# Kernel optimization log

Hardware: AMD Instinct MI355X
Metric: run time of the kernel (lower is better)

The kernel has to match this reference:

```python
import jax, jax.numpy as jnp
import numpy as np

COORD = 2
C_IN = 64
C_OUT = 4
PROJ_HID = 256
N_LAT = 4096
N_QRY = 16384
B = 4
E0 = 262144
E1 = 524288
KERNEL_DIMS = [2 * COORD, 64, 64, C_IN]  # LinearChannelMLP layers for the GNO kernel


def _init_linear(key, d_in, d_out):
    kw, kb = jax.random.split(key)
    scale = 1.0 / np.sqrt(d_in)
    W = jax.random.uniform(kw, (d_in, d_out), jnp.float32, -scale, scale)
    b = jax.random.uniform(kb, (d_out,), jnp.float32, -scale, scale)
    return W, b


def setup_inputs() -> dict:
    key = jax.random.key(0)
    ks = jax.random.split(key, 16)
    inp = {
        "latent_tokens_coord": jax.random.uniform(ks[0], (N_LAT, COORD), jnp.float32),
        "rndata": jax.random.normal(ks[1], (B, N_LAT, C_IN), jnp.float32),
        "query_coord": jax.random.uniform(ks[2], (N_QRY, COORD), jnp.float32),
        "src0": jax.random.randint(ks[3], (E0,), 0, N_LAT, jnp.int32),
        "qry0": jnp.sort(jax.random.randint(ks[4], (E0,), 0, N_QRY, jnp.int32)),
        "src1": jax.random.randint(ks[5], (E1,), 0, N_LAT, jnp.int32),
        "qry1": jnp.sort(jax.random.randint(ks[6], (E1,), 0, N_QRY, jnp.int32)),
    }
    # GNO kernel MLP (shared across scales): 4 -> 64 -> 64 -> 64, GELU between layers
    for i in range(3):
        W, b = _init_linear(ks[7 + i], KERNEL_DIMS[i], KERNEL_DIMS[i + 1])
        inp[f"Wk{i}"], inp[f"bk{i}"] = W, b
    # scale-weighting MLP: coord_dim -> 16 -> num_scales, softmax over scales
    inp["Wsw0"], inp["bsw0"] = _init_linear(ks[10], COORD, 16)
    inp["Wsw1"], inp["bsw1"] = _init_linear(ks[11], 16, 2)
    # projection ChannelMLP: in_channels -> 256 -> out_channels, GELU between
    inp["Wp0"], inp["bp0"] = _init_linear(ks[12], C_IN, PROJ_HID)
    inp["Wp1"], inp["bp1"] = _init_linear(ks[13], PROJ_HID, C_OUT)
    return inp


def _kernel_mlp(feat, Wk0, bk0, Wk1, bk1, Wk2, bk2):
    h = jax.nn.gelu(feat @ Wk0 + bk0)
    h = jax.nn.gelu(h @ Wk1 + bk1)
    return h @ Wk2 + bk2  # [E, C_IN]


def _gno_scale(latent_coord, query_coord, rndata, src, qry,
               Wk0, bk0, Wk1, bk1, Wk2, bk2):
    # gather per-edge coords: agg = cat(y_j, x_i) -> kernel MLP -> linear transform k * f_y
    feat = jnp.concatenate([latent_coord[src], query_coord[qry]], axis=-1)  # [E, 2*COORD]
    k = _kernel_mlp(feat, Wk0, bk0, Wk1, bk1, Wk2, bk2)                     # [E, C_IN]
    fy = rndata[:, src, :]                                                  # [B, E, C_IN]
    m = (k[None, :, :] * fy).transpose(1, 0, 2)                             # [E, B, C_IN]
    s = jax.ops.segment_sum(m, qry, num_segments=N_QRY)                     # [Q, B, C_IN]
    cnt = jax.ops.segment_sum(jnp.ones_like(qry, dtype=m.dtype), qry, num_segments=N_QRY)
    mean = s / jnp.maximum(cnt, 1.0)[:, None, None]                         # mean reduction
    return mean.transpose(1, 0, 2)                                          # [B, Q, C_IN]


def reference(latent_tokens_coord, rndata, query_coord,
              src0, qry0, src1, qry1,
              Wk0, bk0, Wk1, bk1, Wk2, bk2,
              Wsw0, bsw0, Wsw1, bsw1,
              Wp0, bp0, Wp1, bp1):
    d0 = _gno_scale(latent_tokens_coord, query_coord, rndata, src0, qry0,
                    Wk0, bk0, Wk1, bk1, Wk2, bk2)
    d1 = _gno_scale(latent_tokens_coord, query_coord, rndata, src1, qry1,
                    Wk0, bk0, Wk1, bk1, Wk2, bk2)
    # scale weights from query coords: softmax over scales
    h = jax.nn.relu(query_coord @ Wsw0 + bsw0)
    w = jax.nn.softmax(h @ Wsw1 + bsw1, axis=-1)          # [Q, 2]
    decoded = w[None, :, 0, None] * d0 + w[None, :, 1, None] * d1  # [B, Q, C_IN]
    # projection ChannelMLP (pointwise over nodes)
    out = jax.nn.gelu(decoded @ Wp0 + bp0) @ Wp1 + bp1    # [B, Q, C_OUT]
    return out
```

## Files before the change

kernel.cpp:

```cpp
#include <hip/hip_runtime.h>
#include <hip/hip_bf16.h>
#include <cstdint>

#define NLAT 4096
#define NQRY 16384
#define QPW  2
#define HSTR 68

#define WSYNC() asm volatile("s_waitcnt lgkmcnt(0)" ::: "memory")

typedef __attribute__((ext_vector_type(8))) short bh8;
typedef __attribute__((ext_vector_type(4))) float f32x4;

union FI { int i[4]; bh8 v; };

__device__ __forceinline__ float gelu_f(float x) {
    float x3 = x * x * x;
    float u2 = 1.5957691216057308f * (x + 0.044715f * x3);
    float r  = __builtin_amdgcn_rcpf(__expf(u2) + 1.0f);
    return x * (1.0f - r);
}

__device__ __forceinline__ int lower_bound(const int* __restrict__ a, int n, int v) {
    int lo = 0, hi = n;
    while (lo < hi) { int m = (lo + hi) >> 1; if (a[m] < v) lo = m + 1; else hi = m; }
    return lo;
}

__device__ __forceinline__ int pk(float a, float b) {
    return (int)__builtin_amdgcn_perm(__float_as_uint(b), __float_as_uint(a), 0x07060302u);
}

__device__ __forceinline__ void make_afrags(const float* sh, int lane, FI ah[2], FI al[2]) {
    const int m = lane & 15, quad = lane >> 4;
#pragma unroll
    for (int ks = 0; ks < 2; ks++) {
        const float* p = sh + m * HSTR + ks * 32 + quad * 8;
        float4 v0 = *(const float4*)p;
        float4 v1 = *(const float4*)(p + 4);
        float x[8] = {v0.x, v0.y, v0.z, v0.w, v1.x, v1.y, v1.z, v1.w};
#pragma unroll
        for (int jj = 0; jj < 4; jj++) {
            float a = x[2 * jj], b = x[2 * jj + 1];
            ah[ks].i[jj] = pk(a, b);
            float la = a - __uint_as_float(__float_as_uint(a) & 0xFFFF0000u);
            float lb = b - __uint_as_float(__float_as_uint(b) & 0xFFFF0000u);
            al[ks].i[jj] = pk(la, lb);
        }
    }
}

__global__ __launch_bounds__(64, 2) void fused_kernel(
    const float* __restrict__ lat,  const float* __restrict__ rnd,
    const float* __restrict__ qc,
    const int* __restrict__ src0, const int* __restrict__ qry0, int E0,
    const int* __restrict__ src1, const int* __restrict__ qry1, int E1,
    const float* __restrict__ Wk0, const float* __restrict__ bk0,
    const float* __restrict__ Wk1, const float* __restrict__ bk1,
    const float* __restrict__ Wk2, const float* __restrict__ bk2,
    const float* __restrict__ Wsw0, const float* __restrict__ bsw0,
    const float* __restrict__ Wsw1, const float* __restrict__ bsw1,
    const float* __restrict__ Wp0, const float* __restrict__ bp0,
    const float* __restrict__ Wp1, const float* __restrict__ bp1,
    float* __restrict__ out)
{
    const int lane = threadIdx.x;
    const int m16  = lane & 15;
    const int quad = lane >> 4;

    __shared__ __align__(16) float sh[16 * HSTR];
    __shared__ __align__(16) float decs[4][64];

    FI wh[2][2][4], wl[2][2][4];
    {
        const float* Wmat[2] = {Wk1, Wk2};
#pragma unroll
        for (int L = 0; L < 2; L++)
#pragma unroll
            for (int ks = 0; ks < 2; ks++)
#pragma unroll
                for (int nt = 0; nt < 4; nt++)
#pragma unroll
                    for (int jj = 0; jj < 4; jj++) {
                        int k0 = ks * 32 + quad * 8 + 2 * jj;
                        float a = Wmat[L][(size_t)k0 * 64 + nt * 16 + m16];
                        float b = Wmat[L][(size_t)(k0 + 1) * 64 + nt * 16 + m16];
                        wh[L][ks][nt].i[jj] = pk(a, b);
                        float la = a - __uint_as_float(__float_as_uint(a) & 0xFFFF0000u);
                        float lb = b - __uint_as_float(__float_as_uint(b) & 0xFFFF0000u);
                        wl[L][ks][nt].i[jj] = pk(la, lb);
                    }
    }

    const float w00 = Wk0[0 * 64 + lane];
    const float w01 = Wk0[1 * 64 + lane];
    const float w02 = Wk0[2 * 64 + lane];
    const float w03 = Wk0[3 * 64 + lane];
    const float b0  = bk0[lane];
    float b1v[4], b2v[4];
#pragma unroll
    for (int nt = 0; nt < 4; nt++) {
        b1v[nt] = bk1[16 * nt + m16];
        b2v[nt] = bk2[16 * nt + m16];
    }

    const int qbase = blockIdx.x * QPW;
    int bs = 0;
    {
        const bool in0 = lane < 3;
        const bool act = lane < 6;
        const int* arr = in0 ? qry0 : qry1;
        const int  n   = in0 ? E0 : E1;
        const int  v   = qbase + (in0 ? lane : lane - 3);
        if (act) bs = lower_bound(arr, n, v);
    }

    for (int qi = 0; qi < QPW; qi++) {
        const int q = qbase + qi;
        const float qc0 = qc[2 * q];
        const float qc1 = qc[2 * q + 1];
        const float base0 = b0 + qc0 * w02 + qc1 * w03;

        const int lo0 = __shfl(bs, qi, 64),     hi0 = __shfl(bs, qi + 1, 64);
        const int lo1 = __shfl(bs, 3 + qi, 64), hi1 = __shfl(bs, 4 + qi, 64);

        float msum[2][4];

#pragma unroll
        for (int set = 0; set < 2; set++) {
            const int* __restrict__ srcp = set ? src1 : src0;
            const int lo = set ? lo1 : lo0;
            const int hi = set ? hi1 : hi0;
            float a0 = 0.f, a1 = 0.f, a2 = 0.f, a3 = 0.f;

            int curS = 0; float curl0 = 0.f, curl1 = 0.f;
            if (lo < hi) {
                int idx = lo + m16; if (idx >= hi) idx = hi - 1;
                curS  = srcp[idx];
                curl0 = lat[2 * curS];
                curl1 = lat[2 * curS + 1];
            }

            for (int e0 = lo; e0 < hi; e0 += 16) {
                const int rem = min(16, hi - e0);

                int nS = 0; float nl0 = 0.f, nl1 = 0.f;
                if (e0 + 16 < hi) {
                    int idx = e0 + 16 + m16; if (idx >= hi) idx = hi - 1;
                    nS  = srcp[idx];
                    nl0 = lat[2 * nS];
                    nl1 = lat[2 * nS + 1];
                }

#pragma unroll
                for (int e = 0; e < 16; e++) {
                    float l0 = __shfl(curl0, e, 64);
                    float l1 = __shfl(curl1, e, 64);
                    sh[e * HSTR + lane] = gelu_f(base0 + l0 * w00 + l1 * w01);
                }
                WSYNC();

                FI ah[2], al[2];
                make_afrags(sh, lane, ah, al);
                WSYNC();

#pragma unroll
                for (int nt = 0; nt < 4; nt++) {
                    f32x4 C = {0.f, 0.f, 0.f, 0.f};
#pragma unroll
                    for (int ks = 0; ks < 2; ks++) {
                        C = __builtin_amdgcn_mfma_f32_16x16x32_bf16(ah[ks].v, wh[0][ks][nt].v, C, 0, 0, 0);
                        C = __builtin_amdgcn_mfma_f32_16x16x32_bf16(al[ks].v, wh[0][ks][nt].v, C, 0, 0, 0);
                        C = __builtin_amdgcn_mfma_f32_16x16x32_bf16(ah[ks].v, wl[0][ks][nt].v, C, 0, 0, 0);
                    }
#pragma unroll
                    for (int r = 0; r < 4; r++)
                        sh[(quad * 4 + r) * HSTR + 16 * nt + m16] = gelu_f(C[r] + b1v[nt]);
                }
                WSYNC();

                float rA[8][4];
#pragma unroll
                for (int e = 0; e < 8; e++) {
                    const int s = __shfl(curS, e, 64);
                    const float* rp = rnd + (size_t)s * 64 + lane;
                    rA[e][0] = rp[0];
                    rA[e][1] = rp[(size_t)1 * NLAT * 64];
                    rA[e][2] = rp[(size_t)2 * NLAT * 64];
                    rA[e][3] = rp[(size_t)3 * NLAT * 64];
                }

                make_afrags(sh, lane, ah, al);
                WSYNC();

#pragma unroll
                for (int nt = 0; nt < 4; nt++) {
                    f32x4 C = {0.f, 0.f, 0.f, 0.f};
#pragma unroll
                    for (int ks = 0; ks < 2; ks++) {
                        C = __builtin_amdgcn_mfma_f32_16x16x32_bf16(ah[ks].v, wh[1][ks][nt].v, C, 0, 0, 0);
                        C = __builtin_amdgcn_mfma_f32_16x16x32_bf16(al[ks].v, wh[1][ks][nt].v, C, 0, 0, 0);
                        C = __builtin_amdgcn_mfma_f32_16x16x32_bf16(ah[ks].v, wl[1][ks][nt].v, C, 0, 0, 0);
                    }
#pragma unroll
                    for (int r = 0; r < 4; r++)
                        sh[(quad * 4 + r) * HSTR + 16 * nt + m16] = C[r] + b2v[nt];
                }
                WSYNC();

                float kvv[16];
#pragma unroll
                for (int e = 0; e < 16; e++) {
                    const float v = sh[e * HSTR + lane];
                    kvv[e] = (e < rem) ? v : 0.f;
                }

                float rB[8][4];
#pragma unroll
                for (int e = 0; e < 8; e++) {
                    const int s = __shfl(curS, 8 + e, 64);
                    const float* rp = rnd + (size_t)s * 64 + lane;
                    rB[e][0] = rp[0];
                    rB[e][1] = rp[(size_t)1 * NLAT * 64];
                    rB[e][2] = rp[(size_t)2 * NLAT * 64];
                    rB[e][3] = rp[(size_t)3 * NLAT * 64];
                }

#pragma unroll
                for (int e = 0; e < 8; e++) {
                    a0 += kvv[e] * rA[e][0];
                    a1 += kvv[e] * rA[e][1];
                    a2 += kvv[e] * rA[e][2];
                    a3 += kvv[e] * rA[e][3];
                }
#pragma unroll
                for (int e = 0; e < 8; e++) {
                    a0 += kvv[8 + e] * rB[e][0];
                    a1 += kvv[8 + e] * rB[e][1];
                    a2 += kvv[8 + e] * rB[e][2];
                    a3 += kvv[8 + e] * rB[e][3];
                }
                WSYNC();

                curS = nS; curl0 = nl0; curl1 = nl1;
            }

            const float scale = __builtin_amdgcn_rcpf(fmaxf((float)(hi - lo), 1.0f));
            msum[set][0] = a0 * scale; msum[set][1] = a1 * scale;
            msum[set][2] = a2 * scale; msum[set][3] = a3 * scale;
        }

        float z0 = bsw1[0], z1 = bsw1[1];
#pragma unroll
        for (int i = 0; i < 16; i++) {
            const float h = fmaxf(0.f, qc0 * Wsw0[i] + qc1 * Wsw0[16 + i] + bsw0[i]);
            z0 += h * Wsw1[i * 2 + 0];
            z1 += h * Wsw1[i * 2 + 1];
        }
        const float zm = fmaxf(z0, z1);
        const float e0s = __expf(z0 - zm), e1s = __expf(z1 - zm);
        const float inv = __builtin_amdgcn_rcpf(e0s + e1s);
        const float g0 = e0s * inv, g1 = e1s * inv;

        WSYNC();
#pragma unroll
        for (int b = 0; b < 4; b++) decs[b][lane] = g0 * msum[0][b] + g1 * msum[1][b];
        WSYNC();

        float hacc[4][4];
        {
            const float4 bv = ((const float4*)bp0)[lane];
            const float bt[4] = { bv.x, bv.y, bv.z, bv.w };
#pragma unroll
            for (int t = 0; t < 4; t++)
#pragma unroll
                for (int b = 0; b < 4; b++) hacc[t][b] = bt[t];
        }
#pragma unroll 8
        for (int c = 0; c < 64; c++) {
            const float4 w = ((const float4*)Wp0)[c * 64 + lane];
            const float wf[4] = { w.x, w.y, w.z, w.w };
            const float d0 = decs[0][c], d1 = decs[1][c], d2 = decs[2][c], d3 = decs[3][c];
#pragma unroll
            for (int t = 0; t < 4; t++) {
                hacc[t][0] += wf[t] * d0;
                hacc[t][1] += wf[t] * d1;
                hacc[t][2] += wf[t] * d2;
                hacc[t][3] += wf[t] * d3;
            }
        }
#pragma unroll
        for (int t = 0; t < 4; t++)
#pragma unroll
            for (int b = 0; b < 4; b++) hacc[t][b] = gelu_f(hacc[t][b]);

        float po[4][4];
#pragma unroll
        for (int b = 0; b < 4; b++)
#pragma unroll
            for (int k = 0; k < 4; k++) po[b][k] = 0.f;
#pragma unroll
        for (int t = 0; t < 4; t++) {
            const float4 w = ((const float4*)Wp1)[4 * lane + t];
            const float wf[4] = { w.x, w.y, w.z, w.w };
#pragma unroll
            for (int k = 0; k < 4; k++)
#pragma unroll
                for (int b = 0; b < 4; b++) po[b][k] += hacc[t][b] * wf[k];
        }
#pragma unroll
        for (int b = 0; b < 4; b++)
#pragma unroll
            for (int k = 0; k < 4; k++) {
                float v = po[b][k];
#pragma unroll
                for (int off = 32; off >= 1; off >>= 1) v += __shfl_xor(v, off, 64);
                po[b][k] = v;
            }

        if (lane == 0) {
#pragma unroll
            for (int b = 0; b < 4; b++)
#pragma unroll
                for (int k = 0; k < 4; k++)
                    out[((size_t)b * NQRY + q) * 4 + k] = po[b][k] + bp1[k];
        }
        WSYNC();
    }
}

extern "C" void kernel_launch(void* const* d_in, const int* in_sizes, int n_in,
                              void* d_out, int out_size, void* d_ws, size_t ws_size,
                              hipStream_t stream) {
    const float* lat  = (const float*)d_in[0];
    const float* rnd  = (const float*)d_in[1];
    const float* qc   = (const float*)d_in[2];
    const int*   src0 = (const int*)d_in[3];
    const int*   qry0 = (const int*)d_in[4];
    const int*   src1 = (const int*)d_in[5];
    const int*   qry1 = (const int*)d_in[6];
    const float* Wk0 = (const float*)d_in[7],  *bk0 = (const float*)d_in[8];
    const float* Wk1 = (const float*)d_in[9],  *bk1 = (const float*)d_in[10];
    const float* Wk2 = (const float*)d_in[11], *bk2 = (const float*)d_in[12];
    const float* Wsw0 = (const float*)d_in[13], *bsw0 = (const float*)d_in[14];
    const float* Wsw1 = (const float*)d_in[15], *bsw1 = (const float*)d_in[16];
    const float* Wp0 = (const float*)d_in[17], *bp0 = (const float*)d_in[18];
    const float* Wp1 = (const float*)d_in[19], *bp1 = (const float*)d_in[20];

    const int E0 = in_sizes[3];
    const int E1 = in_sizes[5];

    fused_kernel<<<NQRY / QPW, 64, 0, stream>>>(
        lat, rnd, qc, src0, qry0, E0, src1, qry1, E1,
        Wk0, bk0, Wk1, bk1, Wk2, bk2,
        Wsw0, bsw0, Wsw1, bsw1, Wp0, bp0, Wp1, bp1,
        (float*)d_out);
}
```

Baseline: 403.0 us.

## Pack four waves per block, prefetch both edge sets, add lo*lo MFMA term

```diff
diff --git a/kernel.cpp b/kernel.cpp
--- a/kernel.cpp
+++ b/kernel.cpp
@@ -5,6 +5,7 @@
 #define NLAT 4096
 #define NQRY 16384
 #define QPW  2
+#define WPB  4
 #define HSTR 68
 
 #define WSYNC() asm volatile("s_waitcnt lgkmcnt(0)" ::: "memory")
@@ -50,7 +51,7 @@
     }
 }
 
-__global__ __launch_bounds__(64, 2) void fused_kernel(
+__global__ __launch_bounds__(WPB * 64, 4) void fused_kernel(
     const float* __restrict__ lat,  const float* __restrict__ rnd,
     const float* __restrict__ qc,
     const int* __restrict__ src0, const int* __restrict__ qry0, int E0,
@@ -64,12 +65,15 @@
     const float* __restrict__ Wp1, const float* __restrict__ bp1,
     float* __restrict__ out)
 {
-    const int lane = threadIdx.x;
+    const int lane = threadIdx.x & 63;
+    const int wid  = threadIdx.x >> 6;
     const int m16  = lane & 15;
     const int quad = lane >> 4;
 
-    __shared__ __align__(16) float sh[16 * HSTR];
-    __shared__ __align__(16) float decs[4][64];
+    __shared__ __align__(16) float sh_all[WPB][16 * HSTR];
+    __shared__ __align__(16) float decs_all[WPB][4][64];
+    float* __restrict__ sh = sh_all[wid];
+    float (* __restrict__ decs)[64] = decs_all[wid];
 
     FI wh[2][2][4], wl[2][2][4];
     {
@@ -104,7 +108,7 @@
         b2v[nt] = bk2[16 * nt + m16];
     }
 
-    const int qbase = blockIdx.x * QPW;
+    const int qbase = (blockIdx.x * WPB + wid) * QPW;
     int bs = 0;
     {
         const bool in0 = lane < 3;
@@ -124,6 +128,19 @@
         const int lo0 = __shfl(bs, qi, 64),     hi0 = __shfl(bs, qi + 1, 64);
         const int lo1 = __shfl(bs, 3 + qi, 64), hi1 = __shfl(bs, 4 + qi, 64);
 
+        int pS[2] = {0, 0}; float pl0[2] = {0.f, 0.f}, pl1[2] = {0.f, 0.f};
+#pragma unroll
+        for (int s = 0; s < 2; s++) {
+            const int lo = s ? lo1 : lo0, hi = s ? hi1 : hi0;
+            const int* sp = s ? src1 : src0;
+            if (lo < hi) {
+                int idx = lo + m16; if (idx >= hi) idx = hi - 1;
+                pS[s]  = sp[idx];
+                pl0[s] = lat[2 * pS[s]];
+                pl1[s] = lat[2 * pS[s] + 1];
+            }
+        }
+
         float msum[2][4];
 
 #pragma unroll
@@ -133,13 +150,7 @@
             const int hi = set ? hi1 : hi0;
             float a0 = 0.f, a1 = 0.f, a2 = 0.f, a3 = 0.f;
 
-            int curS = 0; float curl0 = 0.f, curl1 = 0.f;
-            if (lo < hi) {
-                int idx = lo + m16; if (idx >= hi) idx = hi - 1;
-                curS  = srcp[idx];
-                curl0 = lat[2 * curS];
-                curl1 = lat[2 * curS + 1];
-            }
+            int curS = pS[set]; float curl0 = pl0[set], curl1 = pl1[set];
 
             for (int e0 = lo; e0 < hi; e0 += 16) {
                 const int rem = min(16, hi - e0);
@@ -172,6 +183,7 @@
                         C = __builtin_amdgcn_mfma_f32_16x16x32_bf16(ah[ks].v, wh[0][ks][nt].v, C, 0, 0, 0);
                         C = __builtin_amdgcn_mfma_f32_16x16x32_bf16(al[ks].v, wh[0][ks][nt].v, C, 0, 0, 0);
                         C = __builtin_amdgcn_mfma_f32_16x16x32_bf16(ah[ks].v, wl[0][ks][nt].v, C, 0, 0, 0);
+                        C = __builtin_amdgcn_mfma_f32_16x16x32_bf16(al[ks].v, wl[0][ks][nt].v, C, 0, 0, 0);
                     }
 #pragma unroll
                     for (int r = 0; r < 4; r++)
@@ -201,18 +213,11 @@
                         C = __builtin_amdgcn_mfma_f32_16x16x32_bf16(ah[ks].v, wh[1][ks][nt].v, C, 0, 0, 0);
                         C = __builtin_amdgcn_mfma_f32_16x16x32_bf16(al[ks].v, wh[1][ks][nt].v, C, 0, 0, 0);
                         C = __builtin_amdgcn_mfma_f32_16x16x32_bf16(ah[ks].v, wl[1][ks][nt].v, C, 0, 0, 0);
+                        C = __builtin_amdgcn_mfma_f32_16x16x32_bf16(al[ks].v, wl[1][ks][nt].v, C, 0, 0, 0);
                     }
 #pragma unroll
                     for (int r = 0; r < 4; r++)
                         sh[(quad * 4 + r) * HSTR + 16 * nt + m16] = C[r] + b2v[nt];
-                }
-                WSYNC();
-
-                float kvv[16];
-#pragma unroll
-                for (int e = 0; e < 16; e++) {
-                    const float v = sh[e * HSTR + lane];
-                    kvv[e] = (e < rem) ? v : 0.f;
                 }
 
                 float rB[8][4];
@@ -224,6 +229,14 @@
                     rB[e][1] = rp[(size_t)1 * NLAT * 64];
                     rB[e][2] = rp[(size_t)2 * NLAT * 64];
                     rB[e][3] = rp[(size_t)3 * NLAT * 64];
+                }
+                WSYNC();
+
+                float kvv[16];
+#pragma unroll
+                for (int e = 0; e < 16; e++) {
+                    const float v = sh[e * HSTR + lane];
+                    kvv[e] = (e < rem) ? v : 0.f;
                 }
 
 #pragma unroll
@@ -350,7 +363,7 @@
     const int E0 = in_sizes[3];
     const int E1 = in_sizes[5];
 
-    fused_kernel<<<NQRY / QPW, 64, 0, stream>>>(
+    fused_kernel<<<NQRY / (QPW * WPB), WPB * 64, 0, stream>>>(
         lat, rnd, qc, src0, qry0, E0, src1, qry1, E1,
         Wk0, bk0, Wk1, bk1, Wk2, bk2,
         Wsw0, bsw0, Wsw1, bsw1, Wp0, bp0, Wp1, bp1,
```

After: 599.9 us. 1.49x slower.
